# Performance work log

Measured on AMD Instinct MI355X. Metric: run time of the kernel, lower is better.

Reference implementation:

```python
import jax, jax.numpy as jnp
import numpy as np

# Dims: B=batch, N_IN=input capsules, D_IN=input capsule dim,
#       J=output capsules (nb_capsules), C=output capsule dim (capsule_size)
B, N_IN, D_IN, J, C = 32, 2048, 16, 64, 32
ITERS = 5
EPS = 1e-7  # K.epsilon()


def squash(v):
    # Keras code: vector += eps; norm = sum(v^2, -1, keepdims); v * norm/(1+norm)/sqrt(norm)
    v = v + EPS
    n = jnp.sum(v * v, axis=-1, keepdims=True)
    return v * (n / (1.0 + n) / jnp.sqrt(n))


def setup_inputs() -> dict:
    key = jax.random.key(0)
    k1, k2 = jax.random.split(key)
    x = jax.random.normal(k1, (B, N_IN, D_IN, 1), dtype=jnp.float32)
    # glorot_uniform over fan_in=D_IN (last axis), fan_out=C
    limit = float(np.sqrt(6.0 / (D_IN + C)))
    W = jax.random.uniform(k2, (N_IN, J, C, D_IN), dtype=jnp.float32,
                           minval=-limit, maxval=limit)
    return {"x": x, "W": W}


def reference(x, W):
    # x: (B, N_IN, D_IN, 1) -> u: (B, N_IN, D_IN)
    u = x[..., 0]
    # Prediction vectors u_hat[b,i,j] = W[i,j] @ u[b,i] : (B, N_IN, J, C)
    u_hat = jnp.einsum('bid,ijcd->bijc', u, W)
    # Routing logits b_ij: (B, N_IN, J)
    b = jnp.zeros(u_hat.shape[:3], dtype=u_hat.dtype)
    v = None
    for i in range(ITERS):
        c = jax.nn.softmax(b, axis=1)              # softmax over input capsules (axis=1 in source)
        s = jnp.einsum('bij,bijc->bjc', c, u_hat)   # weighted sum over i -> (B, J, C)
        v = squash(s)                                # squash over capsule vector dim C
        if i < ITERS - 1:
            # agreement update: b += <v_j, u_hat_ij>
            b = b + jnp.einsum('bjc,bijc->bij', v, u_hat)
    # match compute_output_shape (B, nb_capsules, capsule_size, 1)
    return v[..., None]
```

## Files before the change

kernel.cpp:

```cpp
#include <hip/hip_runtime.h>
#include <hip/hip_bf16.h>

#define B_ 32
#define N_ 2048
#define D_ 16
#define J_ 64
#define C_ 32
#define NCHUNK 32
#define ICHUNK 64
#define IPW    16

typedef __attribute__((ext_vector_type(8)))  short short8;
typedef __attribute__((ext_vector_type(4)))  short s16x4;
typedef __attribute__((ext_vector_type(16))) float f32x16;
typedef __attribute__((ext_vector_type(4)))  float f32x4;
typedef __attribute__((ext_vector_type(16))) int   i32x16;
typedef __attribute__((ext_vector_type(2)))  long  longx2;

using bf16_t = __hip_bfloat16;

__global__ __launch_bounds__(256) void prep_u_kernel(const float* __restrict__ x,
                                                     bf16_t* __restrict__ ut,
                                                     signed char* __restrict__ uq,
                                                     float* __restrict__ su) {
  int t = blockIdx.x * 256 + threadIdx.x;
  int b = t & 31;
  int i = t >> 5;
  const float* xp = x + (size_t)(b * N_ + i) * D_;
  float v[16];
  *(f32x4*)(v)      = *(const f32x4*)(xp);
  *(f32x4*)(v + 4)  = *(const f32x4*)(xp + 4);
  *(f32x4*)(v + 8)  = *(const f32x4*)(xp + 8);
  *(f32x4*)(v + 12) = *(const f32x4*)(xp + 12);

  float m = 0.f;
#pragma unroll
  for (int k = 0; k < 16; ++k) m = fmaxf(m, fabsf(v[k]));
  m = fmaxf(m, 1e-20f);
  float inv = 127.0f / m;
  union { longx2 l2; signed char c[16]; } pk;
#pragma unroll
  for (int k = 0; k < 16; ++k) pk.c[k] = (signed char)__float2int_rn(v[k] * inv);
  *(longx2*)(uq + (size_t)t * D_) = pk.l2;
  su[t] = m * (1.0f / 127.0f);

  union { short8 s; bf16_t h[8]; } o0, o1;
#pragma unroll
  for (int k = 0; k < 8; ++k) { o0.h[k] = __float2bfloat16(v[k]); o1.h[k] = __float2bfloat16(v[8 + k]); }
  *(short8*)(ut + (size_t)t * D_)     = o0.s;
  *(short8*)(ut + (size_t)t * D_ + 8) = o1.s;
}

__global__ __launch_bounds__(256) void prep_w_kernel(const float* __restrict__ Wf,
                                                     signed char* __restrict__ Wq,
                                                     float* __restrict__ SW) {
  const int lane = threadIdx.x & 63;
  const int wid  = (blockIdx.x * 256 + threadIdx.x) >> 6;
  const int nw   = gridDim.x * 4;
  for (int tile = wid; tile < N_ * J_; tile += nw) {
    const float* wp = Wf + (size_t)tile * (C_ * D_) + lane * 8;
    f32x4 a = *(const f32x4*)wp;
    f32x4 b = *(const f32x4*)(wp + 4);
    float wv[8] = {a.x, a.y, a.z, a.w, b.x, b.y, b.z, b.w};
    float m = 0.f;
#pragma unroll
    for (int k = 0; k < 8; ++k) m = fmaxf(m, fabsf(wv[k]));
    m = fmaxf(m, __shfl_xor(m, 1));
    m = fmaxf(m, __shfl_xor(m, 2));
    m = fmaxf(m, __shfl_xor(m, 4));
    m = fmaxf(m, __shfl_xor(m, 8));
    m = fmaxf(m, __shfl_xor(m, 16));
    m = fmaxf(m, __shfl_xor(m, 32));
    m = fmaxf(m, 1e-20f);
    float qs = 127.0f / m;
    union { long l; signed char c[8]; } pk;
#pragma unroll
    for (int k = 0; k < 8; ++k) pk.c[k] = (signed char)__float2int_rn(wv[k] * qs);
    *(long*)(Wq + (size_t)tile * (C_ * D_) + lane * 8) = pk.l;
    if (lane == 0) SW[tile] = m * (1.0f / 127.0f);
  }
}

template<int MODE>
__global__ __launch_bounds__(256) void pass_kernel(
    const float*        __restrict__ Wf,
    const signed char*  __restrict__ Wq,
    const float*        __restrict__ SW,
    const signed char*  __restrict__ uq,
    const float*        __restrict__ su,
    const bf16_t*       __restrict__ ut,
    const float*        __restrict__ V,
    float*              __restrict__ PS,
    float*              __restrict__ PZ)
{
  constexpr bool UNIFORM = (MODE == 0 || MODE == 2);
  constexpr bool INT8    = (MODE == 0 || MODE == 1);

  const int tid  = threadIdx.x;
  const int w    = tid >> 6;
  const int lane = tid & 63;
  const int half = lane >> 5;
  const int lc   = lane & 31;

  const int j  = blockIdx.x / NCHUNK;
  const int ch = blockIdx.x % NCHUNK;

  int crow[16];
#pragma unroll
  for (int r = 0; r < 16; ++r) crow[r] = (r & 3) + 4 * half + 8 * (r >> 2);

  float Vreg[16];
  if (!UNIFORM) {
#pragma unroll
    for (int r = 0; r < 16; ++r) Vreg[r] = V[(lc * J_ + j) * C_ + crow[r]];
  }

  float S[16];
#pragma unroll
  for (int r = 0; r < 16; ++r) S[r] = 0.f;
  float zacc = 0.f;

  const int ibase = ch * ICHUNK + w * IPW;
  const int frag_off = lc * D_ + half * 8;

  if constexpr (INT8) {
    const i32x16 zi = {0,0,0,0,0,0,0,0,0,0,0,0,0,0,0,0};
    long wl = *(const long*)(Wq + ((size_t)ibase * J_ + j) * (C_ * D_) + frag_off);
    long ul = *(const long*)(uq + (size_t)ibase * (B_ * D_) + frag_off);
    float sc = SW[(size_t)ibase * J_ + j] * su[ibase * B_ + lc];

    for (int t = 0; t < IPW; ++t) {
      const int tn = (t + 1 < IPW) ? t + 1 : t;
      const int in_ = ibase + tn;
      long wl_n = *(const long*)(Wq + ((size_t)in_ * J_ + j) * (C_ * D_) + frag_off);
      long ul_n = *(const long*)(uq + (size_t)in_ * (B_ * D_) + frag_off);
      float sc_n = SW[(size_t)in_ * J_ + j] * su[in_ * B_ + lc];

      i32x16 iacc = __builtin_amdgcn_mfma_i32_32x32x16_i8(wl, ul, zi, 0, 0, 0);

      if constexpr (UNIFORM) {
#pragma unroll
        for (int r = 0; r < 16; ++r) S[r] = fmaf(sc, (float)iacc[r], S[r]);
      } else {
        float af[16];
        float ph = 0.f;
#pragma unroll
        for (int r = 0; r < 16; ++r) { af[r] = (float)iacc[r]; ph = fmaf(Vreg[r], af[r], ph); }
        ph *= sc;
        ph += __shfl_xor(ph, 32);
        float e = __expf(ph);
        zacc += e;
        float es = e * sc;
#pragma unroll
        for (int r = 0; r < 16; ++r) S[r] = fmaf(es, af[r], S[r]);
      }
      wl = wl_n; ul = ul_n; sc = sc_n;
    }
  } else {
    const f32x16 zeroacc = {0,0,0,0,0,0,0,0,0,0,0,0,0,0,0,0};
    for (int t = 0; t < IPW; ++t) {
      const int i = ibase + t;
      short8 ufrag = *(const short8*)(ut + (size_t)i * (B_ * D_) + frag_off);
      const size_t tile = ((size_t)i * J_ + j) * (C_ * D_);
      const float* wp = Wf + tile + frag_off;
      f32x4 w0 = *(const f32x4*)(wp);
      f32x4 w1 = *(const f32x4*)(wp + 4);
      union { short8 v; bf16_t h[8]; } cv;
      cv.h[0] = __float2bfloat16(w0.x);
      cv.h[1] = __float2bfloat16(w0.y);
      cv.h[2] = __float2bfloat16(w0.z);
      cv.h[3] = __float2bfloat16(w0.w);
      cv.h[4] = __float2bfloat16(w1.x);
      cv.h[5] = __float2bfloat16(w1.y);
      cv.h[6] = __float2bfloat16(w1.z);
      cv.h[7] = __float2bfloat16(w1.w);
      short8 wfrag = cv.v;

      f32x16 acc = __builtin_amdgcn_mfma_f32_32x32x16_bf16(wfrag, ufrag, zeroacc, 0, 0, 0);

      if constexpr (UNIFORM) {
#pragma unroll
        for (int r = 0; r < 16; ++r) S[r] += acc[r];
      } else {
        float ph = 0.f;
#pragma unroll
        for (int r = 0; r < 16; ++r) ph = fmaf(Vreg[r], acc[r], ph);
        ph += __shfl_xor(ph, 32);
        float e = __expf(ph);
        zacc += e;
#pragma unroll
        for (int r = 0; r < 16; ++r) S[r] = fmaf(e, acc[r], S[r]);
      }
    }
  }

  __shared__ float S_lds[4 * 32 * 33];
  __shared__ float Z_lds[4 * 32];
#pragma unroll
  for (int r = 0; r < 16; ++r)
    S_lds[w * 1056 + lc * 33 + crow[r]] = S[r];
  if (!half)
    Z_lds[w * 32 + lc] = UNIFORM ? (float)IPW : zacc;
  __syncthreads();

  const size_t pbase = (size_t)blockIdx.x * 1024;
  for (int e = tid; e < 1024; e += 256) {
    int b = e >> 5, c = e & 31;
    PS[pbase + e] = S_lds[b * 33 + c] + S_lds[1056 + b * 33 + c] +
                    S_lds[2112 + b * 33 + c] + S_lds[3168 + b * 33 + c];
  }
  if (tid < 32)
    PZ[(size_t)blockIdx.x * 32 + tid] =
        Z_lds[tid] + Z_lds[32 + tid] + Z_lds[64 + tid] + Z_lds[96 + tid];
}

__global__ __launch_bounds__(256) void combine_kernel(
    const float* __restrict__ PS, const float* __restrict__ PZ,
    float* __restrict__ V, float* __restrict__ out, int first, int last)
{
  int t  = blockIdx.x * 256 + threadIdx.x;
  int c  = t & 31;
  int bj = t >> 5;
  int b  = bj >> 6;
  int j  = bj & 63;
  float s = 0.f, zz = 0.f;
#pragma unroll
  for (int ch = 0; ch < NCHUNK; ++ch) {
    s  += PS[(size_t)(j * NCHUNK + ch) * 1024 + b * 32 + c];
    zz += PZ[(j * NCHUNK + ch) * 32 + b];
  }
  float sv = s / zz + 1e-7f;
  float n = sv * sv;
  n += __shfl_xor(n, 1);
  n += __shfl_xor(n, 2);
  n += __shfl_xor(n, 4);
  n += __shfl_xor(n, 8);
  n += __shfl_xor(n, 16);
  float f = n / ((1.f + n) * sqrtf(n));
  float v = sv * f;
  float Vn = first ? v : (V[t] + v);
  V[t] = Vn;
  if (last) out[t] = v;
}

extern "C" void kernel_launch(void* const* d_in, const int* in_sizes, int n_in,
                              void* d_out, int out_size, void* d_ws, size_t ws_size,
                              hipStream_t stream)
{
  const float* x  = (const float*)d_in[0];
  const float* Wf = (const float*)d_in[1];
  float* out = (float*)d_out;
  char* ws = (char*)d_ws;

  const size_t SZ_WQ = (size_t)N_ * J_ * C_ * D_;
  const size_t SZ_SW = (size_t)N_ * J_ * 4;
  const size_t SZ_UQ = (size_t)N_ * B_ * D_;
  const size_t SZ_SU = (size_t)N_ * B_ * 4;
  const size_t SZ_UT = (size_t)N_ * B_ * D_ * 2;
  const size_t SZ_V  = (size_t)B_ * J_ * C_ * 4;
  const size_t SZ_PS = (size_t)J_ * NCHUNK * B_ * C_ * 4;
  const size_t SZ_PZ = (size_t)J_ * NCHUNK * B_ * 4;

  const bool big = ws_size >= SZ_WQ + SZ_SW + SZ_UQ + SZ_SU + SZ_UT + SZ_V + SZ_PS + SZ_PZ;
  char* p = ws;
  signed char* Wq = nullptr;
  float* SWp = nullptr;
  if (big) {
    Wq  = (signed char*)p; p += SZ_WQ;
    SWp = (float*)p;       p += SZ_SW;
  }
  signed char* uq = (signed char*)p; p += SZ_UQ;
  float* su = (float*)p;             p += SZ_SU;
  bf16_t* ut = (bf16_t*)p;           p += SZ_UT;
  float*  V  = (float*)p;            p += SZ_V;
  float*  PS = (float*)p;            p += SZ_PS;
  float*  PZ = (float*)p;

  prep_u_kernel<<<dim3((N_ * B_) / 256), dim3(256), 0, stream>>>(x, ut, uq, su);

  dim3 gA(J_ * NCHUNK), blk(256), gB((B_ * J_ * C_) / 256);
  if (big) {
    prep_w_kernel<<<dim3(2048), blk, 0, stream>>>(Wf, Wq, SWp);
    pass_kernel<0><<<gA, blk, 0, stream>>>(nullptr, Wq, SWp, uq, su, nullptr, nullptr, PS, PZ);
    combine_kernel<<<gB, blk, 0, stream>>>(PS, PZ, V, out, 1, 0);
    for (int it = 1; it < 5; ++it) {
      pass_kernel<1><<<gA, blk, 0, stream>>>(nullptr, Wq, SWp, uq, su, nullptr, V, PS, PZ);
      combine_kernel<<<gB, blk, 0, stream>>>(PS, PZ, V, out, 0, it == 4 ? 1 : 0);
    }
  } else {
    pass_kernel<2><<<gA, blk, 0, stream>>>(Wf, nullptr, nullptr, uq, su, ut, nullptr, PS, PZ);
    combine_kernel<<<gB, blk, 0, stream>>>(PS, PZ, V, out, 1, 0);
    for (int it = 1; it < 5; ++it) {
      pass_kernel<3><<<gA, blk, 0, stream>>>(Wf, nullptr, nullptr, uq, su, ut, V, PS, PZ);
      combine_kernel<<<gB, blk, 0, stream>>>(PS, PZ, V, out, 0, it == 4 ? 1 : 0);
    }
  }
}
```

Measured before the change: 512.2 us.

## Fuse W quantization into first pass and combine step into next routing pass

The separate W-quantization kernel is folded into the first routing pass, which quantizes W to int8 on the fly, stores it, and uses it directly for the MFMA. This avoids a second full read of the fp32 W. Each later pass now reduces the previous pass's partial sums and applies the squash itself, with ping-pong buffers, so the standalone combine launches go away. Chunks per output capsule drop from 32 to 8, giving 512 blocks with 64 inputs per wave, which cuts partial-sum traffic but lowers parallelism and makes every block redundantly recompute the squash for its capsule.

```diff
diff --git a/kernel.cpp b/kernel.cpp
--- a/kernel.cpp
+++ b/kernel.cpp
@@ -6,12 +6,16 @@
 #define D_ 16
 #define J_ 64
 #define C_ 32
+
+#define NCH8 8
+#define ICH8 256
+#define IPW8 64
+
 #define NCHUNK 32
 #define ICHUNK 64
 #define IPW    16
 
 typedef __attribute__((ext_vector_type(8)))  short short8;
-typedef __attribute__((ext_vector_type(4)))  short s16x4;
 typedef __attribute__((ext_vector_type(16))) float f32x16;
 typedef __attribute__((ext_vector_type(4)))  float f32x4;
 typedef __attribute__((ext_vector_type(16))) int   i32x16;
@@ -51,50 +55,204 @@
   *(short8*)(ut + (size_t)t * D_ + 8) = o1.s;
 }
 
-__global__ __launch_bounds__(256) void prep_w_kernel(const float* __restrict__ Wf,
-                                                     signed char* __restrict__ Wq,
-                                                     float* __restrict__ SW) {
-  const int lane = threadIdx.x & 63;
-  const int wid  = (blockIdx.x * 256 + threadIdx.x) >> 6;
-  const int nw   = gridDim.x * 4;
-  for (int tile = wid; tile < N_ * J_; tile += nw) {
-    const float* wp = Wf + (size_t)tile * (C_ * D_) + lane * 8;
-    f32x4 a = *(const f32x4*)wp;
-    f32x4 b = *(const f32x4*)(wp + 4);
-    float wv[8] = {a.x, a.y, a.z, a.w, b.x, b.y, b.z, b.w};
-    float m = 0.f;
-#pragma unroll
-    for (int k = 0; k < 8; ++k) m = fmaxf(m, fabsf(wv[k]));
-    m = fmaxf(m, __shfl_xor(m, 1));
-    m = fmaxf(m, __shfl_xor(m, 2));
-    m = fmaxf(m, __shfl_xor(m, 4));
-    m = fmaxf(m, __shfl_xor(m, 8));
-    m = fmaxf(m, __shfl_xor(m, 16));
-    m = fmaxf(m, __shfl_xor(m, 32));
-    m = fmaxf(m, 1e-20f);
-    float qs = 127.0f / m;
-    union { long l; signed char c[8]; } pk;
-#pragma unroll
-    for (int k = 0; k < 8; ++k) pk.c[k] = (signed char)__float2int_rn(wv[k] * qs);
-    *(long*)(Wq + (size_t)tile * (C_ * D_) + lane * 8) = pk.l;
-    if (lane == 0) SW[tile] = m * (1.0f / 127.0f);
-  }
+template<int MODE>
+__global__ __launch_bounds__(256, 2) void pass_big_kernel(
+    const float*        __restrict__ Wf,
+    signed char*        __restrict__ Wq,
+    float*              __restrict__ SW,
+    const signed char*  __restrict__ uq,
+    const float*        __restrict__ su,
+    const float*        __restrict__ PSr,
+    const float*        __restrict__ PZr,
+    float*              __restrict__ PSw,
+    float*              __restrict__ PZw,
+    const float*        __restrict__ Vr,
+    float*              __restrict__ Vw,
+    int it)
+{
+  const int tid  = threadIdx.x;
+  const int bid  = blockIdx.x;
+  const int w    = tid >> 6;
+  const int lane = tid & 63;
+  const int half = lane >> 5;
+  const int lc   = lane & 31;
+  const int j    = bid >> 3;
+  const int ch   = bid & 7;
+
+  int crow[16];
+#pragma unroll
+  for (int r = 0; r < 16; ++r) crow[r] = (r & 3) + 4 * half + 8 * (r >> 2);
+
+  __shared__ float S_lds[4 * 32 * 33];
+  __shared__ float Z_lds[4 * 32];
+  __shared__ float V_lds[32 * 33];
+
+  float Vreg[16];
+  if constexpr (MODE == 1) {
+#pragma unroll
+    for (int k = 0; k < 4; ++k) {
+      const int e = tid + k * 256;
+      const int b = e >> 5, c = e & 31;
+      float s = 0.f, z = 0.f;
+#pragma unroll
+      for (int cc = 0; cc < NCH8; ++cc) {
+        s += PSr[(size_t)(j * NCH8 + cc) * 1024 + e];
+        z += PZr[(j * NCH8 + cc) * 32 + b];
+      }
+      float sv = s / z + 1e-7f;
+      float n = sv * sv;
+      n += __shfl_xor(n, 1);
+      n += __shfl_xor(n, 2);
+      n += __shfl_xor(n, 4);
+      n += __shfl_xor(n, 8);
+      n += __shfl_xor(n, 16);
+      float f = n / ((1.f + n) * sqrtf(n));
+      float v = sv * f;
+      float Vs = (it == 1) ? v : (Vr[((size_t)b * J_ + j) * C_ + c] + v);
+      Vw[((size_t)b * J_ + j) * C_ + c] = Vs;
+      V_lds[b * 33 + c] = Vs;
+    }
+    __syncthreads();
+#pragma unroll
+    for (int r = 0; r < 16; ++r) Vreg[r] = V_lds[lc * 33 + crow[r]];
+  }
+
+  const int ibase    = ch * ICH8 + w * IPW8;
+  const int frag_off = lc * D_ + half * 8;
+
+  float S[16];
+#pragma unroll
+  for (int r = 0; r < 16; ++r) S[r] = 0.f;
+  float zacc = 0.f;
+  const i32x16 zi = {0,0,0,0,0,0,0,0,0,0,0,0,0,0,0,0};
+
+  if constexpr (MODE == 0) {
+    const size_t t0 = ((size_t)ibase * J_ + j) * (C_ * D_) + frag_off;
+    f32x4 w0 = *(const f32x4*)(Wf + t0);
+    f32x4 w1 = *(const f32x4*)(Wf + t0 + 4);
+    long  ul = *(const long*)(uq + (size_t)ibase * (B_ * D_) + frag_off);
+    float suv = su[ibase * B_ + lc];
+
+    for (int t = 0; t < IPW8; ++t) {
+      const int i   = ibase + t;
+      const int tn  = (t + 1 < IPW8) ? t + 1 : t;
+      const int in_ = ibase + tn;
+      const size_t tn_off = ((size_t)in_ * J_ + j) * (C_ * D_) + frag_off;
+      f32x4 w0n = *(const f32x4*)(Wf + tn_off);
+      f32x4 w1n = *(const f32x4*)(Wf + tn_off + 4);
+      long  uln = *(const long*)(uq + (size_t)in_ * (B_ * D_) + frag_off);
+      float sun = su[in_ * B_ + lc];
+
+      float wv[8] = {w0.x, w0.y, w0.z, w0.w, w1.x, w1.y, w1.z, w1.w};
+      float m = 0.f;
+#pragma unroll
+      for (int k = 0; k < 8; ++k) m = fmaxf(m, fabsf(wv[k]));
+      m = fmaxf(m, __shfl_xor(m, 1));
+      m = fmaxf(m, __shfl_xor(m, 2));
+      m = fmaxf(m, __shfl_xor(m, 4));
+      m = fmaxf(m, __shfl_xor(m, 8));
+      m = fmaxf(m, __shfl_xor(m, 16));
+      m = fmaxf(m, __shfl_xor(m, 32));
+      m = fmaxf(m, 1e-20f);
+      float qs = 127.0f / m;
+      union { long l; signed char c[8]; } pk;
+#pragma unroll
+      for (int k = 0; k < 8; ++k) pk.c[k] = (signed char)__float2int_rn(wv[k] * qs);
+      const size_t tile = ((size_t)i * J_ + j) * (C_ * D_);
+      *(long*)(Wq + tile + frag_off) = pk.l;
+      float swv = m * (1.0f / 127.0f);
+      if (lane == 0) SW[(size_t)i * J_ + j] = swv;
+      float sc_ = swv * suv;
+
+      i32x16 iacc = __builtin_amdgcn_mfma_i32_32x32x16_i8(pk.l, ul, zi, 0, 0, 0);
+#pragma unroll
+      for (int r = 0; r < 16; ++r) S[r] = fmaf(sc_, (float)iacc[r], S[r]);
+
+      w0 = w0n; w1 = w1n; ul = uln; suv = sun;
+    }
+  } else {
+    long  wl = *(const long*)(Wq + ((size_t)ibase * J_ + j) * (C_ * D_) + frag_off);
+    long  ul = *(const long*)(uq + (size_t)ibase * (B_ * D_) + frag_off);
+    float sc = SW[(size_t)ibase * J_ + j] * su[ibase * B_ + lc];
+
+    for (int t = 0; t < IPW8; ++t) {
+      const int tn  = (t + 1 < IPW8) ? t + 1 : t;
+      const int in_ = ibase + tn;
+      long  wl_n = *(const long*)(Wq + ((size_t)in_ * J_ + j) * (C_ * D_) + frag_off);
+      long  ul_n = *(const long*)(uq + (size_t)in_ * (B_ * D_) + frag_off);
+      float sc_n = SW[(size_t)in_ * J_ + j] * su[in_ * B_ + lc];
+
+      i32x16 iacc = __builtin_amdgcn_mfma_i32_32x32x16_i8(wl, ul, zi, 0, 0, 0);
+
+      float af[16];
+      float ph = 0.f;
+#pragma unroll
+      for (int r = 0; r < 16; ++r) { af[r] = (float)iacc[r]; ph = fmaf(Vreg[r], af[r], ph); }
+      ph *= sc;
+      ph += __shfl_xor(ph, 32);
+      float e = __expf(ph);
+      zacc += e;
+      float es = e * sc;
+#pragma unroll
+      for (int r = 0; r < 16; ++r) S[r] = fmaf(es, af[r], S[r]);
+
+      wl = wl_n; ul = ul_n; sc = sc_n;
+    }
+  }
+
+#pragma unroll
+  for (int r = 0; r < 16; ++r)
+    S_lds[w * 1056 + lc * 33 + crow[r]] = S[r];
+  if (!half)
+    Z_lds[w * 32 + lc] = (MODE == 0) ? (float)IPW8 : zacc;
+  __syncthreads();
+
+  const size_t pbase = (size_t)bid * 1024;
+  for (int e = tid; e < 1024; e += 256) {
+    int b = e >> 5, c = e & 31;
+    PSw[pbase + e] = S_lds[b * 33 + c] + S_lds[1056 + b * 33 + c] +
+                     S_lds[2112 + b * 33 + c] + S_lds[3168 + b * 33 + c];
+  }
+  if (tid < 32)
+    PZw[bid * 32 + tid] =
+        Z_lds[tid] + Z_lds[32 + tid] + Z_lds[64 + tid] + Z_lds[96 + tid];
+}
+
+__global__ __launch_bounds__(256) void combine_final_kernel(
+    const float* __restrict__ PS, const float* __restrict__ PZ,
+    float* __restrict__ out)
+{
+  int t  = blockIdx.x * 256 + threadIdx.x;
+  int c  = t & 31;
+  int bj = t >> 5;
+  int b  = bj >> 6;
+  int j  = bj & 63;
+  float s = 0.f, z = 0.f;
+#pragma unroll
+  for (int cc = 0; cc < NCH8; ++cc) {
+    s += PS[(size_t)(j * NCH8 + cc) * 1024 + b * 32 + c];
+    z += PZ[(j * NCH8 + cc) * 32 + b];
+  }
+  float sv = s / z + 1e-7f;
+  float n = sv * sv;
+  n += __shfl_xor(n, 1);
+  n += __shfl_xor(n, 2);
+  n += __shfl_xor(n, 4);
+  n += __shfl_xor(n, 8);
+  n += __shfl_xor(n, 16);
+  float f = n / ((1.f + n) * sqrtf(n));
+  out[t] = sv * f;
 }
 
 template<int MODE>
 __global__ __launch_bounds__(256) void pass_kernel(
     const float*        __restrict__ Wf,
-    const signed char*  __restrict__ Wq,
-    const float*        __restrict__ SW,
-    const signed char*  __restrict__ uq,
-    const float*        __restrict__ su,
     const bf16_t*       __restrict__ ut,
     const float*        __restrict__ V,
     float*              __restrict__ PS,
     float*              __restrict__ PZ)
 {
-  constexpr bool UNIFORM = (MODE == 0 || MODE == 2);
-  constexpr bool INT8    = (MODE == 0 || MODE == 1);
+  constexpr bool UNIFORM = (MODE == 2);
 
   const int tid  = threadIdx.x;
   const int w    = tid >> 6;
@@ -123,74 +281,39 @@
   const int ibase = ch * ICHUNK + w * IPW;
   const int frag_off = lc * D_ + half * 8;
 
-  if constexpr (INT8) {
-    const i32x16 zi = {0,0,0,0,0,0,0,0,0,0,0,0,0,0,0,0};
-    long wl = *(const long*)(Wq + ((size_t)ibase * J_ + j) * (C_ * D_) + frag_off);
-    long ul = *(const long*)(uq + (size_t)ibase * (B_ * D_) + frag_off);
-    float sc = SW[(size_t)ibase * J_ + j] * su[ibase * B_ + lc];
-
-    for (int t = 0; t < IPW; ++t) {
-      const int tn = (t + 1 < IPW) ? t + 1 : t;
-      const int in_ = ibase + tn;
-      long wl_n = *(const long*)(Wq + ((size_t)in_ * J_ + j) * (C_ * D_) + frag_off);
-      long ul_n = *(const long*)(uq + (size_t)in_ * (B_ * D_) + frag_off);
-      float sc_n = SW[(size_t)in_ * J_ + j] * su[in_ * B_ + lc];
-
-      i32x16 iacc = __builtin_amdgcn_mfma_i32_32x32x16_i8(wl, ul, zi, 0, 0, 0);
-
-      if constexpr (UNIFORM) {
-#pragma unroll
-        for (int r = 0; r < 16; ++r) S[r] = fmaf(sc, (float)iacc[r], S[r]);
-      } else {
-        float af[16];
-        float ph = 0.f;
-#pragma unroll
-        for (int r = 0; r < 16; ++r) { af[r] = (float)iacc[r]; ph = fmaf(Vreg[r], af[r], ph); }
-        ph *= sc;
-        ph += __shfl_xor(ph, 32);
-        float e = __expf(ph);
-        zacc += e;
-        float es = e * sc;
-#pragma unroll
-        for (int r = 0; r < 16; ++r) S[r] = fmaf(es, af[r], S[r]);
-      }
-      wl = wl_n; ul = ul_n; sc = sc_n;
-    }
-  } else {
-    const f32x16 zeroacc = {0,0,0,0,0,0,0,0,0,0,0,0,0,0,0,0};
-    for (int t = 0; t < IPW; ++t) {
-      const int i = ibase + t;
-      short8 ufrag = *(const short8*)(ut + (size_t)i * (B_ * D_) + frag_off);
-      const size_t tile = ((size_t)i * J_ + j) * (C_ * D_);
-      const float* wp = Wf + tile + frag_off;
-      f32x4 w0 = *(const f32x4*)(wp);
-      f32x4 w1 = *(const f32x4*)(wp + 4);
-      union { short8 v; bf16_t h[8]; } cv;
-      cv.h[0] = __float2bfloat16(w0.x);
-      cv.h[1] = __float2bfloat16(w0.y);
-      cv.h[2] = __float2bfloat16(w0.z);
-      cv.h[3] = __float2bfloat16(w0.w);
-      cv.h[4] = __float2bfloat16(w1.x);
-      cv.h[5] = __float2bfloat16(w1.y);
-      cv.h[6] = __float2bfloat16(w1.z);
-      cv.h[7] = __float2bfloat16(w1.w);
-      short8 wfrag = cv.v;
-
-      f32x16 acc = __builtin_amdgcn_mfma_f32_32x32x16_bf16(wfrag, ufrag, zeroacc, 0, 0, 0);
-
-      if constexpr (UNIFORM) {
-#pragma unroll
-        for (int r = 0; r < 16; ++r) S[r] += acc[r];
-      } else {
-        float ph = 0.f;
-#pragma unroll
-        for (int r = 0; r < 16; ++r) ph = fmaf(Vreg[r], acc[r], ph);
-        ph += __shfl_xor(ph, 32);
-        float e = __expf(ph);
-        zacc += e;
-#pragma unroll
-        for (int r = 0; r < 16; ++r) S[r] = fmaf(e, acc[r], S[r]);
-      }
+  const f32x16 zeroacc = {0,0,0,0,0,0,0,0,0,0,0,0,0,0,0,0};
+  for (int t = 0; t < IPW; ++t) {
+    const int i = ibase + t;
+    short8 ufrag = *(const short8*)(ut + (size_t)i * (B_ * D_) + frag_off);
+    const size_t tile = ((size_t)i * J_ + j) * (C_ * D_);
+    const float* wp = Wf + tile + frag_off;
+    f32x4 w0 = *(const f32x4*)(wp);
+    f32x4 w1 = *(const f32x4*)(wp + 4);
+    union { short8 v; bf16_t h[8]; } cv;
+    cv.h[0] = __float2bfloat16(w0.x);
+    cv.h[1] = __float2bfloat16(w0.y);
+    cv.h[2] = __float2bfloat16(w0.z);
+    cv.h[3] = __float2bfloat16(w0.w);
+    cv.h[4] = __float2bfloat16(w1.x);
+    cv.h[5] = __float2bfloat16(w1.y);
+    cv.h[6] = __float2bfloat16(w1.z);
+    cv.h[7] = __float2bfloat16(w1.w);
+    short8 wfrag = cv.v;
+
+    f32x16 acc = __builtin_amdgcn_mfma_f32_32x32x16_bf16(wfrag, ufrag, zeroacc, 0, 0, 0);
+
+    if constexpr (UNIFORM) {
+#pragma unroll
+      for (int r = 0; r < 16; ++r) S[r] += acc[r];
+    } else {
+      float ph = 0.f;
+#pragma unroll
+      for (int r = 0; r < 16; ++r) ph = fmaf(Vreg[r], acc[r], ph);
+      ph += __shfl_xor(ph, 32);
+      float e = __expf(ph);
+      zacc += e;
+#pragma unroll
+      for (int r = 0; r < 16; ++r) S[r] = fmaf(e, acc[r], S[r]);
     }
   }
 
@@ -252,47 +375,69 @@
   float* out = (float*)d_out;
   char* ws = (char*)d_ws;
 
-  const size_t SZ_WQ = (size_t)N_ * J_ * C_ * D_;
-  const size_t SZ_SW = (size_t)N_ * J_ * 4;
-  const size_t SZ_UQ = (size_t)N_ * B_ * D_;
-  const size_t SZ_SU = (size_t)N_ * B_ * 4;
-  const size_t SZ_UT = (size_t)N_ * B_ * D_ * 2;
-  const size_t SZ_V  = (size_t)B_ * J_ * C_ * 4;
-  const size_t SZ_PS = (size_t)J_ * NCHUNK * B_ * C_ * 4;
-  const size_t SZ_PZ = (size_t)J_ * NCHUNK * B_ * 4;
-
-  const bool big = ws_size >= SZ_WQ + SZ_SW + SZ_UQ + SZ_SU + SZ_UT + SZ_V + SZ_PS + SZ_PZ;
-  char* p = ws;
-  signed char* Wq = nullptr;
-  float* SWp = nullptr;
+  const size_t SZ_WQ  = (size_t)N_ * J_ * C_ * D_;
+  const size_t SZ_SW  = (size_t)N_ * J_ * 4;
+  const size_t SZ_UQ  = (size_t)N_ * B_ * D_;
+  const size_t SZ_SU  = (size_t)N_ * B_ * 4;
+  const size_t SZ_UT  = (size_t)N_ * B_ * D_ * 2;
+  const size_t SZ_V   = (size_t)B_ * J_ * C_ * 4;
+  const size_t SZ_PS8 = (size_t)J_ * NCH8 * B_ * C_ * 4;
+  const size_t SZ_PZ8 = (size_t)J_ * NCH8 * B_ * 4;
+  const size_t SZ_PSF = (size_t)J_ * NCHUNK * B_ * C_ * 4;
+  const size_t SZ_PZF = (size_t)J_ * NCHUNK * B_ * 4;
+
+  const size_t need_big = SZ_WQ + SZ_SW + SZ_UQ + SZ_SU + SZ_UT +
+                          2 * SZ_V + 2 * SZ_PS8 + 2 * SZ_PZ8;
+  const bool big = ws_size >= need_big;
+
+  dim3 blk(256);
+
   if (big) {
-    Wq  = (signed char*)p; p += SZ_WQ;
-    SWp = (float*)p;       p += SZ_SW;
-  }
-  signed char* uq = (signed char*)p; p += SZ_UQ;
-  float* su = (float*)p;             p += SZ_SU;
-  bf16_t* ut = (bf16_t*)p;           p += SZ_UT;
-  float*  V  = (float*)p;            p += SZ_V;
-  float*  PS = (float*)p;            p += SZ_PS;
-  float*  PZ = (float*)p;
-
-  prep_u_kernel<<<dim3((N_ * B_) / 256), dim3(256), 0, stream>>>(x, ut, uq, su);
-
-  dim3 gA(J_ * NCHUNK), blk(256), gB((B_ * J_ * C_) / 256);
-  if (big) {
-    prep_w_kernel<<<dim3(2048), blk, 0, stream>>>(Wf, Wq, SWp);
-    pass_kernel<0><<<gA, blk, 0, stream>>>(nullptr, Wq, SWp, uq, su, nullptr, nullptr, PS, PZ);
+    char* p = ws;
+    signed char* Wq = (signed char*)p; p += SZ_WQ;
+    float* SWp = (float*)p;            p += SZ_SW;
+    signed char* uq = (signed char*)p; p += SZ_UQ;
+    float* su = (float*)p;             p += SZ_SU;
+    bf16_t* ut = (bf16_t*)p;           p += SZ_UT;
+    float* V0  = (float*)p;            p += SZ_V;
+    float* V1  = (float*)p;            p += SZ_V;
+    float* PS0 = (float*)p;            p += SZ_PS8;
+    float* PS1 = (float*)p;            p += SZ_PS8;
+    float* PZ0 = (float*)p;            p += SZ_PZ8;
+    float* PZ1 = (float*)p;
+
+    prep_u_kernel<<<dim3((N_ * B_) / 256), blk, 0, stream>>>(x, ut, uq, su);
+
+    pass_big_kernel<0><<<dim3(J_ * NCH8), blk, 0, stream>>>(
+        Wf, Wq, SWp, uq, su, nullptr, nullptr, PS0, PZ0, V0, V0, 0);
+
+    for (int it = 1; it < 5; ++it) {
+      float* psw = (it & 1) ? PS1 : PS0;
+      float* pzw = (it & 1) ? PZ1 : PZ0;
+      const float* psr = (it & 1) ? PS0 : PS1;
+      const float* pzr = (it & 1) ? PZ0 : PZ1;
+      float* vw = (it & 1) ? V1 : V0;
+      const float* vr = (it & 1) ? V0 : V1;
+      pass_big_kernel<1><<<dim3(J_ * NCH8), blk, 0, stream>>>(
+          nullptr, Wq, SWp, uq, su, psr, pzr, psw, pzw, vr, vw, it);
+    }
+    combine_final_kernel<<<dim3((B_ * J_ * C_) / 256), blk, 0, stream>>>(PS0, PZ0, out);
+  } else {
+    char* p = ws;
+    signed char* uq = (signed char*)p; p += SZ_UQ;
+    float* su = (float*)p;             p += SZ_SU;
+    bf16_t* ut = (bf16_t*)p;           p += SZ_UT;
+    float*  V  = (float*)p;            p += SZ_V;
+    float*  PS = (float*)p;            p += SZ_PSF;
+    float*  PZ = (float*)p;
+
+    dim3 gA(J_ * NCHUNK), gB((B_ * J_ * C_) / 256);
+    prep_u_kernel<<<dim3((N_ * B_) / 256), blk, 0, stream>>>(x, ut, uq, su);
+    pass_kernel<2><<<gA, blk, 0, stream>>>(Wf, ut, nullptr, PS, PZ);
     combine_kernel<<<gB, blk, 0, stream>>>(PS, PZ, V, out, 1, 0);
     for (int it = 1; it < 5; ++it) {
-      pass_kernel<1><<<gA, blk, 0, stream>>>(nullptr, Wq, SWp, uq, su, nullptr, V, PS, PZ);
+      pass_kernel<3><<<gA, blk, 0, stream>>>(Wf, ut, V, PS, PZ);
       combine_kernel<<<gB, blk, 0, stream>>>(PS, PZ, V, out, 0, it == 4 ? 1 : 0);
     }
-  } else {
-    pass_kernel<2><<<gA, blk, 0, stream>>>(Wf, nullptr, nullptr, uq, su, ut, nullptr, PS, PZ);
-    combine_kernel<<<gB, blk, 0, stream>>>(PS, PZ, V, out, 1, 0);
-    for (int it = 1; it < 5; ++it) {
-      pass_kernel<3><<<gA, blk, 0, stream>>>(Wf, nullptr, nullptr, uq, su, ut, V, PS, PZ);
-      combine_kernel<<<gB, blk, 0, stream>>>(PS, PZ, V, out, 0, it == 4 ? 1 : 0);
-    }
-  }
-}
+  }
+}
```

Result: slower. 531.8 us (+3.8%).
